# Kernel tuning notes

Hardware: AMD Instinct MI355X
Metric: run time of the kernel (lower is better)

## Reference

```python
import jax, jax.numpy as jnp
import numpy as np

U = 100000   # num_users
I = 100000   # num_items
D = 64       # latent_dim_rec
L = 3        # lightGCN_n_layers
E = 6400000  # number of nonzeros in the sparse adjacency
B = 16384    # batch of (user, item) pairs
N = U + I


def setup_inputs() -> dict:
    key = jax.random.key(0)
    ks = jax.random.split(key, 11)
    return {
        "user_emb": 0.1 * jax.random.normal(ks[0], (U, D), dtype=jnp.float32),
        "item_emb": 0.1 * jax.random.normal(ks[1], (I, D), dtype=jnp.float32),
        "symptom_emb": 0.1 * jax.random.normal(ks[2], (U, D), dtype=jnp.float32),
        "herb_emb": 0.1 * jax.random.normal(ks[3], (I, D), dtype=jnp.float32),
        "user_lw": jax.random.uniform(ks[4], (L + 1,), dtype=jnp.float32),
        "item_lw": jax.random.uniform(ks[5], (L + 1,), dtype=jnp.float32),
        # symmetric-normalized adjacency values are small positive numbers
        "edge_val": jax.random.uniform(ks[6], (E,), dtype=jnp.float32) / 32.0,
        "edge_row": jax.random.randint(ks[7], (E,), 0, N, dtype=jnp.int32),
        "edge_col": jax.random.randint(ks[8], (E,), 0, N, dtype=jnp.int32),
        "users": jax.random.randint(ks[9], (B,), 0, U, dtype=jnp.int32),
        "items": jax.random.randint(ks[10], (B,), 0, I, dtype=jnp.int32),
    }


def _computer(user_emb, item_emb, symptom_emb, herb_emb, user_lw, item_lw,
              edge_val, edge_row, edge_col):
    # layer-0 semantic fusion
    a0 = jax.nn.sigmoid(user_lw[0])
    b0 = jax.nn.sigmoid(item_lw[0])
    u = a0 * user_emb + (1.0 - a0) * symptom_emb
    it = b0 * item_emb + (1.0 - b0) * herb_emb
    all_emb = jnp.concatenate([u, it], axis=0)  # [N, D]
    acc = all_emb  # running sum over layers (mean taken at the end)
    for layer in range(1, L + 1):
        # SpMM: A @ all_emb via gather + segment_sum over edge list
        msg = edge_val[:, None] * all_emb[edge_col]          # [E, D]
        all_emb = jax.ops.segment_sum(msg, edge_row, num_segments=N)
        a = jax.nn.sigmoid(user_lw[layer])
        b = jax.nn.sigmoid(item_lw[layer])
        cu = a * all_emb[:U] + (1.0 - a) * symptom_emb
        ci = b * all_emb[U:] + (1.0 - b) * herb_emb
        all_emb = jnp.concatenate([cu, ci], axis=0)
        acc = acc + all_emb
    light_out = acc / (L + 1)   # mean over stacked layer outputs
    return light_out[:U], light_out[U:]


def reference(user_emb, item_emb, symptom_emb, herb_emb, user_lw, item_lw,
              edge_val, edge_row, edge_col, users, items):
    all_users, all_items = _computer(user_emb, item_emb, symptom_emb, herb_emb,
                                     user_lw, item_lw, edge_val, edge_row, edge_col)
    users_emb = all_users[users]   # [B, D]
    items_emb = all_items[items]   # [B, D]
    gamma = jnp.sum(users_emb * items_emb, axis=1)  # [B]
    return gamma
```

## Files before the change

### kernel.cpp

```cpp
#include <hip/hip_runtime.h>

constexpr int U_N = 100000;
constexpr int I_N = 100000;
constexpr int D   = 64;
constexpr int NL  = 3;
constexpr int NN  = U_N + I_N;
constexpr long long NDLL = (long long)NN * D;
constexpr long long ND4  = NDLL / 4;
constexpr long long UD4  = (long long)U_N * D / 4;

constexpr int BKT_SHIFT = 10;
constexpr int BKT_W     = 1024;
constexpr int NBKT      = (NN + BKT_W - 1) / BKT_W;
constexpr int KSTAGE    = 13;
constexpr int SCHUNK_MAX = KSTAGE * 1024;

typedef float f32x2 __attribute__((ext_vector_type(2)));

__device__ __forceinline__ float sigmoidf_(float x) {
    return 1.0f / (1.0f + expf(-x));
}

__device__ __forceinline__ float bf_lo(unsigned int u) {
    return __uint_as_float(u << 16);
}
__device__ __forceinline__ float bf_hi(unsigned int u) {
    return __uint_as_float(u & 0xFFFF0000u);
}
__device__ __forceinline__ f32x2 bfpair(unsigned int u) {
    f32x2 r;
    r.x = __uint_as_float(u << 16);
    r.y = __uint_as_float(u & 0xFFFF0000u);
    return r;
}
__device__ __forceinline__ unsigned short f2bf(float f) {
    unsigned int u = __float_as_uint(f);
    u += 0x7FFFu + ((u >> 16) & 1u);
    return (unsigned short)(u >> 16);
}
__device__ __forceinline__ unsigned int pack2bf(float lo, float hi) {
    return (unsigned int)f2bf(lo) | ((unsigned int)f2bf(hi) << 16);
}

__global__ void fuse0_bf16_kernel(const float* __restrict__ user_emb,
                                  const float* __restrict__ item_emb,
                                  const float* __restrict__ symptom_emb,
                                  const float* __restrict__ herb_emb,
                                  const float* __restrict__ user_lw,
                                  const float* __restrict__ item_lw,
                                  unsigned short* __restrict__ e0b) {
    long long idx = (long long)blockIdx.x * blockDim.x + threadIdx.x;
    if (idx >= ND4) return;
    float a0 = sigmoidf_(user_lw[0]);
    float b0 = sigmoidf_(item_lw[0]);
    float4 e, s;
    float w;
    if (idx < UD4) {
        e = ((const float4*)user_emb)[idx];
        s = ((const float4*)symptom_emb)[idx];
        w = a0;
    } else {
        long long j = idx - UD4;
        e = ((const float4*)item_emb)[j];
        s = ((const float4*)herb_emb)[j];
        w = b0;
    }
    ushort4 rb;
    rb.x = f2bf(w * e.x + (1.0f - w) * s.x);
    rb.y = f2bf(w * e.y + (1.0f - w) * s.y);
    rb.z = f2bf(w * e.z + (1.0f - w) * s.z);
    rb.w = f2bf(w * e.w + (1.0f - w) * s.w);
    ((ushort4*)e0b)[idx] = rb;
}

__global__ void init_cursor_kernel(int* __restrict__ cursor, int cap) {
    int i = blockIdx.x * blockDim.x + threadIdx.x;
    if (i < NBKT) cursor[i] = i * cap;
}

__global__ void fused_scatter_kernel(const float* __restrict__ edge_val,
                                     const int*   __restrict__ edge_row,
                                     const int*   __restrict__ edge_col,
                                     int* __restrict__ cursor,
                                     int2* __restrict__ binned,
                                     int E, int chunk) {
    __shared__ int h[NBKT];
    int tid = threadIdx.x;
    if (tid < NBKT) h[tid] = 0;
    __syncthreads();
    int s_ = blockIdx.x * chunk;
    int eend = min(E, s_ + chunk);
    int rr[KSTAGE];
    int cc[KSTAGE];
    float vv[KSTAGE];
    #pragma unroll
    for (int k = 0; k < KSTAGE; ++k) {
        int e = s_ + tid + k * 1024;
        bool ok = e < eend;
        rr[k] = ok ? edge_row[e] : -1;
        cc[k] = ok ? edge_col[e] : 0;
        vv[k] = ok ? edge_val[e] : 0.0f;
        if (ok) atomicAdd(&h[rr[k] >> BKT_SHIFT], 1);
    }
    __syncthreads();
    if (tid < NBKT) {
        int c = h[tid];
        if (c) h[tid] = atomicAdd(&cursor[tid], c);
    }
    __syncthreads();
    #pragma unroll
    for (int k = 0; k < KSTAGE; ++k) {
        if (rr[k] >= 0) {
            int b = rr[k] >> BKT_SHIFT;
            int pos = atomicAdd(&h[b], 1);
            binned[pos] = make_int2(__float_as_int(vv[k]),
                                    cc[k] | ((rr[k] & (BKT_W - 1)) << 18));
        }
    }
}

__global__ void bucket_to_csr_kernel(const int2* __restrict__ binned,
                                     const int*  __restrict__ cursor,
                                     int2* __restrict__ row_ptr2,
                                     int2* __restrict__ sorted, int cap) {
    int b = blockIdx.x;
    int start = b * cap;
    int end   = cursor[b];
    __shared__ int rc[BKT_W];
    __shared__ int sm[BKT_W];
    int tid = threadIdx.x;
    rc[tid] = 0;
    __syncthreads();
    for (int e = start + tid; e < end; e += blockDim.x)
        atomicAdd(&rc[(unsigned)binned[e].y >> 18], 1);
    __syncthreads();
    int x = rc[tid];
    sm[tid] = x;
    __syncthreads();
    for (int off = 1; off < BKT_W; off <<= 1) {
        int t = (tid >= off) ? sm[tid - off] : 0;
        __syncthreads();
        sm[tid] += t;
        __syncthreads();
    }
    int excl = sm[tid] - x;
    int gidx = (b << BKT_SHIFT) + tid;
    if (gidx < NN) row_ptr2[gidx] = make_int2(start + excl, start + excl + x);
    __syncthreads();
    rc[tid] = excl;
    __syncthreads();
    for (int e = start + tid; e < end; e += blockDim.x) {
        int2 a = binned[e];
        int rl = (unsigned)a.y >> 18;
        int pos = start + atomicAdd(&rc[rl], 1);
        sorted[pos] = make_int2(a.x, (a.y & 0x3FFFF) << 7);
    }
}

__device__ __forceinline__ void csr_row_sum8(const int2* __restrict__ sorted,
                                             const char* __restrict__ srcB,
                                             int start, int end, unsigned poff,
                                             f32x2 s[4]) {
    #pragma unroll
    for (int j = 0; j < 4; ++j) s[j] = (f32x2){0.f, 0.f};
    int e = start;
    if (e + 8 <= end) {
        int2 a[8];
        #pragma unroll
        for (int k = 0; k < 8; ++k) a[k] = sorted[e + k];
        for (; e + 16 <= end; e += 8) {
            uint4 q[8];
            #pragma unroll
            for (int k = 0; k < 8; ++k)
                q[k] = *(const uint4*)(srcB + (size_t)((unsigned)a[k].y | poff));
            int2 an[8];
            #pragma unroll
            for (int k = 0; k < 8; ++k) an[k] = sorted[e + 8 + k];
            #pragma unroll
            for (int k = 0; k < 8; ++k) {
                f32x2 v; v.x = __int_as_float(a[k].x); v.y = v.x;
                s[0] += v * bfpair(q[k].x);
                s[1] += v * bfpair(q[k].y);
                s[2] += v * bfpair(q[k].z);
                s[3] += v * bfpair(q[k].w);
            }
            #pragma unroll
            for (int k = 0; k < 8; ++k) a[k] = an[k];
        }
        uint4 q[8];
        #pragma unroll
        for (int k = 0; k < 8; ++k)
            q[k] = *(const uint4*)(srcB + (size_t)((unsigned)a[k].y | poff));
        #pragma unroll
        for (int k = 0; k < 8; ++k) {
            f32x2 v; v.x = __int_as_float(a[k].x); v.y = v.x;
            s[0] += v * bfpair(q[k].x);
            s[1] += v * bfpair(q[k].y);
            s[2] += v * bfpair(q[k].z);
            s[3] += v * bfpair(q[k].w);
        }
        e += 8;
    }
    if (e < end) {
        int2 a[8];
        #pragma unroll
        for (int k = 0; k < 8; ++k) {
            int idx = e + k;
            a[k] = sorted[idx < end ? idx : end - 1];
            if (idx >= end) a[k].x = 0;
        }
        uint4 q[8];
        #pragma unroll
        for (int k = 0; k < 8; ++k)
            q[k] = *(const uint4*)(srcB + (size_t)((unsigned)a[k].y | poff));
        #pragma unroll
        for (int k = 0; k < 8; ++k) {
            f32x2 v; v.x = __int_as_float(a[k].x); v.y = v.x;
            s[0] += v * bfpair(q[k].x);
            s[1] += v * bfpair(q[k].y);
            s[2] += v * bfpair(q[k].z);
            s[3] += v * bfpair(q[k].w);
        }
    }
}

__global__ void spmm_csr_full_kernel(const int2* __restrict__ sorted,
                                     const int2* __restrict__ row_ptr2,
                                     const unsigned short* __restrict__ src,
                                     const float* __restrict__ symptom_emb,
                                     const float* __restrict__ herb_emb,
                                     const float* __restrict__ user_lw,
                                     const float* __restrict__ item_lw,
                                     int layer,
                                     unsigned short* __restrict__ dst_b) {
    int wid  = threadIdx.x >> 6;
    int lane = threadIdx.x & 63;
    int r    = lane >> 3;
    int p    = lane & 7;
    int row  = (blockIdx.x * (blockDim.x >> 6) + wid) * 8 + r;
    if (row >= NN) return;
    int2 rp = row_ptr2[row];

    f32x2 s[4];
    csr_row_sum8(sorted, (const char*)src, rp.x, rp.y, (unsigned)(p << 4), s);

    size_t o = ((size_t)row << 6) + ((size_t)p << 3);
    float wgt;
    const float* semp;
    if (row < U_N) {
        wgt = sigmoidf_(user_lw[layer]);
        semp = symptom_emb + o;
    } else {
        wgt = sigmoidf_(item_lw[layer]);
        semp = herb_emb + o - ((size_t)U_N << 6);
    }
    float4 sa = *(const float4*)semp;
    float4 sb = *(const float4*)(semp + 4);
    float om = 1.0f - wgt;
    uint4 ob;
    ob.x = pack2bf(wgt * s[0].x + om * sa.x, wgt * s[0].y + om * sa.y);
    ob.y = pack2bf(wgt * s[1].x + om * sa.z, wgt * s[1].y + om * sa.w);
    ob.z = pack2bf(wgt * s[2].x + om * sb.x, wgt * s[2].y + om * sb.y);
    ob.w = pack2bf(wgt * s[3].x + om * sb.z, wgt * s[3].y + om * sb.w);
    *(uint4*)(dst_b + o) = ob;
}

__global__ void spmm_csr_compact_kernel(const int2* __restrict__ sorted,
                                        const int2* __restrict__ row_ptr2,
                                        const unsigned short* __restrict__ src,
                                        const float* __restrict__ user_emb,
                                        const float* __restrict__ item_emb,
                                        const float* __restrict__ symptom_emb,
                                        const float* __restrict__ herb_emb,
                                        const float* __restrict__ user_lw,
                                        const float* __restrict__ item_lw,
                                        int layer,
                                        const int* __restrict__ users,
                                        const int* __restrict__ items,
                                        const unsigned short* __restrict__ e1b,
                                        const unsigned short* __restrict__ e2b,
                                        float* __restrict__ e3c,
                                        int B) {
    int wid  = threadIdx.x >> 6;
    int lane = threadIdx.x & 63;
    int r    = lane >> 3;
    int p    = lane & 7;
    int b    = (blockIdx.x * (blockDim.x >> 6) + wid) * 8 + r;
    if (b >= 2 * B) return;
    int row = (b < B) ? users[b] : (items[b - B] + U_N);
    int2 rp = row_ptr2[row];

    f32x2 s[4];
    csr_row_sum8(sorted, (const char*)src, rp.x, rp.y, (unsigned)(p << 4), s);

    size_t orow = ((size_t)row << 6) + ((size_t)p << 3);
    float wgt, w0;
    const float* semp;
    const float* embp;
    if (row < U_N) {
        wgt = sigmoidf_(user_lw[layer]);
        w0  = sigmoidf_(user_lw[0]);
        semp = symptom_emb + orow;
        embp = user_emb + orow;
    } else {
        size_t ol = orow - ((size_t)U_N << 6);
        wgt = sigmoidf_(item_lw[layer]);
        w0  = sigmoidf_(item_lw[0]);
        semp = herb_emb + ol;
        embp = item_emb + ol;
    }
    float4 sa = *(const float4*)semp;
    float4 sb = *(const float4*)(semp + 4);
    float4 ea = *(const float4*)embp;
    float4 eb = *(const float4*)(embp + 4);
    uint4 q1 = ((const uint4*)e1b)[((size_t)row << 3) + p];
    uint4 q2 = ((const uint4*)e2b)[((size_t)row << 3) + p];
    float om = 1.0f - wgt, om0 = 1.0f - w0;
    float4 ra, rb;
    ra.x = (w0 * ea.x + om0 * sa.x) + bf_lo(q1.x) + bf_lo(q2.x)
         + (wgt * s[0].x + om * sa.x);
    ra.y = (w0 * ea.y + om0 * sa.y) + bf_hi(q1.x) + bf_hi(q2.x)
         + (wgt * s[0].y + om * sa.y);
    ra.z = (w0 * ea.z + om0 * sa.z) + bf_lo(q1.y) + bf_lo(q2.y)
         + (wgt * s[1].x + om * sa.z);
    ra.w = (w0 * ea.w + om0 * sa.w) + bf_hi(q1.y) + bf_hi(q2.y)
         + (wgt * s[1].y + om * sa.w);
    rb.x = (w0 * eb.x + om0 * sb.x) + bf_lo(q1.z) + bf_lo(q2.z)
         + (wgt * s[2].x + om * sb.x);
    rb.y = (w0 * eb.y + om0 * sb.y) + bf_hi(q1.z) + bf_hi(q2.z)
         + (wgt * s[2].y + om * sb.y);
    rb.z = (w0 * eb.z + om0 * sb.z) + bf_lo(q1.w) + bf_lo(q2.w)
         + (wgt * s[3].x + om * sb.z);
    rb.w = (w0 * eb.w + om0 * sb.w) + bf_hi(q1.w) + bf_hi(q2.w)
         + (wgt * s[3].y + om * sb.w);
    float* op = e3c + ((size_t)b << 6) + ((size_t)p << 3);
    *(float4*)op = ra;
    *(float4*)(op + 4) = rb;
}

__global__ void gamma_kernel(const float* __restrict__ e3c,
                             float* __restrict__ out,
                             int B) {
    int gtid = blockIdx.x * blockDim.x + threadIdx.x;
    int wid  = gtid >> 6;
    int lane = threadIdx.x & 63;
    if (wid >= B) return;
    float su = e3c[((size_t)wid << 6) | lane];
    float si = e3c[((size_t)(B + wid) << 6) | lane];
    float pr = su * si;
    #pragma unroll
    for (int off = 32; off > 0; off >>= 1)
        pr += __shfl_down(pr, off, 64);
    if (lane == 0) out[wid] = pr * (1.0f / 16.0f);
}

__global__ void fuse0_kernel(const float* __restrict__ user_emb,
                             const float* __restrict__ item_emb,
                             const float* __restrict__ symptom_emb,
                             const float* __restrict__ herb_emb,
                             const float* __restrict__ user_lw,
                             const float* __restrict__ item_lw,
                             float* __restrict__ bufA,
                             float* __restrict__ acc,
                             float* __restrict__ bufB) {
    long long idx = (long long)blockIdx.x * blockDim.x + threadIdx.x;
    if (idx >= ND4) return;
    float a0 = sigmoidf_(user_lw[0]);
    float b0 = sigmoidf_(item_lw[0]);
    float4 e, s;
    float w;
    if (idx < UD4) {
        e = ((const float4*)user_emb)[idx];
        s = ((const float4*)symptom_emb)[idx];
        w = a0;
    } else {
        long long j = idx - UD4;
        e = ((const float4*)item_emb)[j];
        s = ((const float4*)herb_emb)[j];
        w = b0;
    }
    float4 r;
    r.x = w * e.x + (1.0f - w) * s.x;
    r.y = w * e.y + (1.0f - w) * s.y;
    r.z = w * e.z + (1.0f - w) * s.z;
    r.w = w * e.w + (1.0f - w) * s.w;
    ((float4*)bufA)[idx] = r;
    ((float4*)acc)[idx]  = r;
    float4 z; z.x = z.y = z.z = z.w = 0.0f;
    ((float4*)bufB)[idx] = z;
}

__global__ void spmm_scatter_kernel(const float* __restrict__ edge_val,
                                    const int*   __restrict__ edge_row,
                                    const int*   __restrict__ edge_col,
                                    const float* __restrict__ src,
                                    float*       __restrict__ dst,
                                    long long total) {
    long long idx = (long long)blockIdx.x * blockDim.x + threadIdx.x;
    if (idx >= total) return;
    long long e = idx >> 4;
    int       q = (int)(idx & 15);
    int r = edge_row[e];
    int c = edge_col[e];
    float v = edge_val[e];
    float4 x = *(const float4*)(src + (long long)c * D + q * 4);
    float* d = dst + (long long)r * D + q * 4;
    atomicAdd(d + 0, v * x.x);
    atomicAdd(d + 1, v * x.y);
    atomicAdd(d + 2, v * x.z);
    atomicAdd(d + 3, v * x.w);
}

__global__ void fuse_layer_kernel(const float* __restrict__ symptom_emb,
                                  const float* __restrict__ herb_emb,
                                  const float* __restrict__ user_lw,
                                  const float* __restrict__ item_lw,
                                  int layer,
                                  float* __restrict__ bufA,
                                  float* __restrict__ bufB,
                                  float* __restrict__ acc) {
    long long idx = (long long)blockIdx.x * blockDim.x + threadIdx.x;
    if (idx >= ND4) return;
    float a = sigmoidf_(user_lw[layer]);
    float b = sigmoidf_(item_lw[layer]);
    float4 m = ((float4*)bufB)[idx];
    float4 z; z.x = z.y = z.z = z.w = 0.0f;
    ((float4*)bufB)[idx] = z;
    float4 s;
    float w;
    if (idx < UD4) {
        s = ((const float4*)symptom_emb)[idx];
        w = a;
    } else {
        s = ((const float4*)herb_emb)[idx - UD4];
        w = b;
    }
    float4 r;
    r.x = w * m.x + (1.0f - w) * s.x;
    r.y = w * m.y + (1.0f - w) * s.y;
    r.z = w * m.z + (1.0f - w) * s.z;
    r.w = w * m.w + (1.0f - w) * s.w;
    ((float4*)bufA)[idx] = r;
    float4 ac = ((float4*)acc)[idx];
    ac.x += r.x; ac.y += r.y; ac.z += r.z; ac.w += r.w;
    ((float4*)acc)[idx] = ac;
}

__global__ void gamma_acc_kernel(const float* __restrict__ acc,
                                 const int* __restrict__ users,
                                 const int* __restrict__ items,
                                 float* __restrict__ out,
                                 int B) {
    int gtid = blockIdx.x * blockDim.x + threadIdx.x;
    int wid  = gtid >> 6;
    int lane = threadIdx.x & 63;
    if (wid >= B) return;
    int u  = users[wid];
    int it = items[wid];
    float su = acc[(long long)u * D + lane];
    float si = acc[((long long)(U_N + it)) * D + lane];
    float p = su * si;
    #pragma unroll
    for (int off = 32; off > 0; off >>= 1)
        p += __shfl_down(p, off, 64);
    if (lane == 0) out[wid] = p * (1.0f / 16.0f);
}

extern "C" void kernel_launch(void* const* d_in, const int* in_sizes, int n_in,
                              void* d_out, int out_size, void* d_ws, size_t ws_size,
                              hipStream_t stream) {
    const float* user_emb    = (const float*)d_in[0];
    const float* item_emb    = (const float*)d_in[1];
    const float* symptom_emb = (const float*)d_in[2];
    const float* herb_emb    = (const float*)d_in[3];
    const float* user_lw     = (const float*)d_in[4];
    const float* item_lw     = (const float*)d_in[5];
    const float* edge_val    = (const float*)d_in[6];
    const int*   edge_row    = (const int*)d_in[7];
    const int*   edge_col    = (const int*)d_in[8];
    const int*   users       = (const int*)d_in[9];
    const int*   items       = (const int*)d_in[10];
    float* out = (float*)d_out;

    const int E = in_sizes[6];
    const int B = in_sizes[9];
    const int TPB = 256;

    int ablk2 = (E + 12499) / 12500;
    int chunk = (E + ablk2 - 1) / ablk2;
    int cap = E / NBKT + E / NBKT / 16 + 1024;
    size_t slab_bytes = (size_t)NBKT * cap * 8;

    size_t off = 0;
    auto carve = [&](size_t bytes) -> char* {
        char* p = (char*)d_ws + off;
        off += (bytes + 255) & ~(size_t)255;
        return p;
    };
    unsigned short* e0b     = (unsigned short*)carve(NDLL * 2);
    unsigned short* e1b     = (unsigned short*)carve(NDLL * 2);
    int2*           binned  = (int2*)carve(slab_bytes);
    int2*           sorted  = (int2*)carve(slab_bytes);
    int2*           row_ptr2= (int2*)carve((size_t)NN * 8);
    int*            cursor  = (int*)carve((size_t)NBKT * 4);
    const size_t fast_bytes = off;
    unsigned short* e2b = e0b;
    float*          e3c = (float*)binned;

    if (ws_size >= fast_bytes && slab_bytes >= (size_t)2 * B * D * 4
        && chunk <= SCHUNK_MAX) {
        int fb = (int)((ND4 + TPB - 1) / TPB);
        fuse0_bf16_kernel<<<fb, TPB, 0, stream>>>(user_emb, item_emb, symptom_emb,
                                                  herb_emb, user_lw, item_lw, e0b);

        init_cursor_kernel<<<1, 256, 0, stream>>>(cursor, cap);
        fused_scatter_kernel<<<ablk2, 1024, 0, stream>>>(edge_val, edge_row,
                                                         edge_col, cursor,
                                                         binned, E, chunk);
        bucket_to_csr_kernel<<<NBKT, BKT_W, 0, stream>>>(binned, cursor,
                                                         row_ptr2, sorted, cap);

        int sblocks = (NN + 31) / 32;
        spmm_csr_full_kernel<<<sblocks, TPB, 0, stream>>>(
            sorted, row_ptr2, e0b, symptom_emb, herb_emb,
            user_lw, item_lw, 1, e1b);
        spmm_csr_full_kernel<<<sblocks, TPB, 0, stream>>>(
            sorted, row_ptr2, e1b, symptom_emb, herb_emb,
            user_lw, item_lw, 2, e2b);
        int cblocks = (2 * B + 31) / 32;
        spmm_csr_compact_kernel<<<cblocks, TPB, 0, stream>>>(
            sorted, row_ptr2, e2b, user_emb, item_emb, symptom_emb, herb_emb,
            user_lw, item_lw, 3, users, items, e1b, e2b, e3c, B);

        int gblocks = (B * 64 + TPB - 1) / TPB;
        gamma_kernel<<<gblocks, TPB, 0, stream>>>(e3c, out, B);
    } else {
        float* bufA = (float*)d_ws;
        float* bufB = bufA + NDLL;
        float* acc2 = bufB + NDLL;

        int fb = (int)((ND4 + TPB - 1) / TPB);
        fuse0_kernel<<<fb, TPB, 0, stream>>>(user_emb, item_emb, symptom_emb,
                                             herb_emb, user_lw, item_lw,
                                             bufA, acc2, bufB);
        for (int layer = 1; layer <= NL; ++layer) {
            long long total = (long long)E * 16;
            int blocks = (int)((total + TPB - 1) / TPB);
            spmm_scatter_kernel<<<blocks, TPB, 0, stream>>>(edge_val, edge_row,
                                                            edge_col, bufA, bufB,
                                                            total);
            int fblocks = (int)((ND4 + TPB - 1) / TPB);
            fuse_layer_kernel<<<fblocks, TPB, 0, stream>>>(symptom_emb, herb_emb,
                                                           user_lw, item_lw, layer,
                                                           bufA, bufB, acc2);
        }
        int gblocks = (B * 64 + TPB - 1) / TPB;
        gamma_acc_kernel<<<gblocks, TPB, 0, stream>>>(acc2, users, items, out, B);
    }
}
```

Measured before the change: 571.3 us.

## Order SpMM rows by descending degree via a counting-sort permutation

```diff
diff --git a/kernel.cpp b/kernel.cpp
--- a/kernel.cpp
+++ b/kernel.cpp
@@ -14,6 +14,7 @@
 constexpr int NBKT      = (NN + BKT_W - 1) / BKT_W;
 constexpr int KSTAGE    = 13;
 constexpr int SCHUNK_MAX = KSTAGE * 1024;
+constexpr int DBINS     = 1024;
 
 typedef float f32x2 __attribute__((ext_vector_type(2)));
 
@@ -154,6 +155,70 @@
         int rl = (unsigned)a.y >> 18;
         int pos = start + atomicAdd(&rc[rl], 1);
         sorted[pos] = make_int2(a.x, (a.y & 0x3FFFF) << 7);
+    }
+}
+
+__global__ void zero_hist_kernel(int* __restrict__ hist) {
+    hist[threadIdx.x] = 0;
+}
+
+__global__ void deg_hist_kernel(const int2* __restrict__ row_ptr2,
+                                int* __restrict__ hist) {
+    __shared__ int h[DBINS];
+    int tid = threadIdx.x;
+    h[tid] = 0;
+    __syncthreads();
+    int i = blockIdx.x * 1024 + tid;
+    if (i < NN) {
+        int2 rp = row_ptr2[i];
+        int d = min(rp.y - rp.x, DBINS - 1);
+        atomicAdd(&h[DBINS - 1 - d], 1);
+    }
+    __syncthreads();
+    int c = h[tid];
+    if (c) atomicAdd(&hist[tid], c);
+}
+
+__global__ void scan_hist_kernel(const int* __restrict__ hist,
+                                 int* __restrict__ cur) {
+    __shared__ int sm[DBINS];
+    int tid = threadIdx.x;
+    int x = hist[tid];
+    sm[tid] = x;
+    __syncthreads();
+    for (int off = 1; off < DBINS; off <<= 1) {
+        int t = (tid >= off) ? sm[tid - off] : 0;
+        __syncthreads();
+        sm[tid] += t;
+        __syncthreads();
+    }
+    cur[tid] = sm[tid] - x;
+}
+
+__global__ void perm_scatter_kernel(const int2* __restrict__ row_ptr2,
+                                    int* __restrict__ cur,
+                                    int* __restrict__ perm) {
+    __shared__ int h[DBINS];
+    __shared__ int base_[DBINS];
+    int tid = threadIdx.x;
+    h[tid] = 0;
+    __syncthreads();
+    int i = blockIdx.x * 1024 + tid;
+    int bin = -1;
+    if (i < NN) {
+        int2 rp = row_ptr2[i];
+        int d = min(rp.y - rp.x, DBINS - 1);
+        bin = DBINS - 1 - d;
+        atomicAdd(&h[bin], 1);
+    }
+    __syncthreads();
+    int c = h[tid];
+    base_[tid] = c ? atomicAdd(&cur[tid], c) : 0;
+    h[tid] = 0;
+    __syncthreads();
+    if (i < NN) {
+        int loc = atomicAdd(&h[bin], 1);
+        perm[base_[bin] + loc] = i;
     }
 }
 
@@ -226,6 +291,7 @@
 
 __global__ void spmm_csr_full_kernel(const int2* __restrict__ sorted,
                                      const int2* __restrict__ row_ptr2,
+                                     const int*  __restrict__ perm,
                                      const unsigned short* __restrict__ src,
                                      const float* __restrict__ symptom_emb,
                                      const float* __restrict__ herb_emb,
@@ -237,9 +303,10 @@
     int lane = threadIdx.x & 63;
     int r    = lane >> 3;
     int p    = lane & 7;
-    int row  = (blockIdx.x * (blockDim.x >> 6) + wid) * 8 + r;
-    if (row >= NN) return;
-    int2 rp = row_ptr2[row];
+    int slot = (blockIdx.x * (blockDim.x >> 6) + wid) * 8 + r;
+    if (slot >= NN) return;
+    int row  = perm[slot];
+    int2 rp  = row_ptr2[row];
 
     f32x2 s[4];
     csr_row_sum8(sorted, (const char*)src, rp.x, rp.y, (unsigned)(p << 4), s);
@@ -503,6 +570,9 @@
     int2*           sorted  = (int2*)carve(slab_bytes);
     int2*           row_ptr2= (int2*)carve((size_t)NN * 8);
     int*            cursor  = (int*)carve((size_t)NBKT * 4);
+    int*            perm    = (int*)carve((size_t)NN * 4);
+    int*            dhist   = (int*)carve((size_t)DBINS * 4);
+    int*            dcur    = (int*)carve((size_t)DBINS * 4);
     const size_t fast_bytes = off;
     unsigned short* e2b = e0b;
     float*          e3c = (float*)binned;
@@ -520,12 +590,18 @@
         bucket_to_csr_kernel<<<NBKT, BKT_W, 0, stream>>>(binned, cursor,
                                                          row_ptr2, sorted, cap);
 
+        int pblocks = (NN + 1023) / 1024;
+        zero_hist_kernel<<<1, DBINS, 0, stream>>>(dhist);
+        deg_hist_kernel<<<pblocks, 1024, 0, stream>>>(row_ptr2, dhist);
+        scan_hist_kernel<<<1, DBINS, 0, stream>>>(dhist, dcur);
+        perm_scatter_kernel<<<pblocks, 1024, 0, stream>>>(row_ptr2, dcur, perm);
+
         int sblocks = (NN + 31) / 32;
         spmm_csr_full_kernel<<<sblocks, TPB, 0, stream>>>(
-            sorted, row_ptr2, e0b, symptom_emb, herb_emb,
+            sorted, row_ptr2, perm, e0b, symptom_emb, herb_emb,
             user_lw, item_lw, 1, e1b);
         spmm_csr_full_kernel<<<sblocks, TPB, 0, stream>>>(
-            sorted, row_ptr2, e1b, symptom_emb, herb_emb,
+            sorted, row_ptr2, perm, e1b, symptom_emb, herb_emb,
             user_lw, item_lw, 2, e2b);
         int cblocks = (2 * B + 31) / 32;
         spmm_csr_compact_kernel<<<cblocks, TPB, 0, stream>>>(
```

Measured after the change: 588.6 us. +3.0%, slower.

## Shrink buckets to 256 rows and sort edges in LDS before coalesced CSR write

Applied to the files above, without the earlier changes.

```diff
diff --git a/kernel.cpp b/kernel.cpp
--- a/kernel.cpp
+++ b/kernel.cpp
@@ -9,9 +9,10 @@
 constexpr long long ND4  = NDLL / 4;
 constexpr long long UD4  = (long long)U_N * D / 4;
 
-constexpr int BKT_SHIFT = 10;
-constexpr int BKT_W     = 1024;
+constexpr int BKT_SHIFT = 8;
+constexpr int BKT_W     = 256;
 constexpr int NBKT      = (NN + BKT_W - 1) / BKT_W;
+constexpr int CAP_MAX   = 9216;
 constexpr int KSTAGE    = 13;
 constexpr int SCHUNK_MAX = KSTAGE * 1024;
 
@@ -123,37 +124,49 @@
                                      const int*  __restrict__ cursor,
                                      int2* __restrict__ row_ptr2,
                                      int2* __restrict__ sorted, int cap) {
+    __shared__ int2 eds[CAP_MAX];
+    __shared__ int  inv[CAP_MAX];
+    __shared__ int  rc[BKT_W];
+    __shared__ int  sm[BKT_W];
     int b = blockIdx.x;
     int start = b * cap;
-    int end   = cursor[b];
-    __shared__ int rc[BKT_W];
-    __shared__ int sm[BKT_W];
+    int cnt   = cursor[b] - start;
+    if (cnt > CAP_MAX) cnt = CAP_MAX;
     int tid = threadIdx.x;
-    rc[tid] = 0;
-    __syncthreads();
-    for (int e = start + tid; e < end; e += blockDim.x)
-        atomicAdd(&rc[(unsigned)binned[e].y >> 18], 1);
-    __syncthreads();
-    int x = rc[tid];
-    sm[tid] = x;
+    if (tid < BKT_W) rc[tid] = 0;
+    __syncthreads();
+    for (int i = tid; i < cnt; i += 1024) {
+        int2 a = binned[start + i];
+        eds[i] = a;
+        atomicAdd(&rc[(unsigned)a.y >> 18], 1);
+    }
+    __syncthreads();
+    int x = 0;
+    if (tid < BKT_W) { x = rc[tid]; sm[tid] = x; }
     __syncthreads();
     for (int off = 1; off < BKT_W; off <<= 1) {
-        int t = (tid >= off) ? sm[tid - off] : 0;
+        int t = (tid >= off && tid < BKT_W) ? sm[tid - off] : 0;
         __syncthreads();
-        sm[tid] += t;
+        if (tid < BKT_W) sm[tid] += t;
         __syncthreads();
     }
-    int excl = sm[tid] - x;
-    int gidx = (b << BKT_SHIFT) + tid;
-    if (gidx < NN) row_ptr2[gidx] = make_int2(start + excl, start + excl + x);
-    __syncthreads();
-    rc[tid] = excl;
-    __syncthreads();
-    for (int e = start + tid; e < end; e += blockDim.x) {
-        int2 a = binned[e];
-        int rl = (unsigned)a.y >> 18;
-        int pos = start + atomicAdd(&rc[rl], 1);
-        sorted[pos] = make_int2(a.x, (a.y & 0x3FFFF) << 7);
+    if (tid < BKT_W) {
+        int excl = sm[tid] - x;
+        int gidx = (b << BKT_SHIFT) + tid;
+        if (gidx < NN)
+            row_ptr2[gidx] = make_int2(start + excl, start + excl + x);
+        rc[tid] = excl;
+    }
+    __syncthreads();
+    for (int i = tid; i < cnt; i += 1024) {
+        int rl  = (unsigned)eds[i].y >> 18;
+        int pos = atomicAdd(&rc[rl], 1);
+        inv[pos] = i;
+    }
+    __syncthreads();
+    for (int t_ = tid; t_ < cnt; t_ += 1024) {
+        int2 a = eds[inv[t_]];
+        sorted[start + t_] = make_int2(a.x, (a.y & 0x3FFFF) << 7);
     }
 }
 
@@ -488,7 +501,7 @@
 
     int ablk2 = (E + 12499) / 12500;
     int chunk = (E + ablk2 - 1) / ablk2;
-    int cap = E / NBKT + E / NBKT / 16 + 1024;
+    int cap = E / NBKT + E / NBKT / 32 + 512;
     size_t slab_bytes = (size_t)NBKT * cap * 8;
 
     size_t off = 0;
@@ -508,17 +521,17 @@
     float*          e3c = (float*)binned;
 
     if (ws_size >= fast_bytes && slab_bytes >= (size_t)2 * B * D * 4
-        && chunk <= SCHUNK_MAX) {
+        && chunk <= SCHUNK_MAX && cap <= CAP_MAX) {
         int fb = (int)((ND4 + TPB - 1) / TPB);
         fuse0_bf16_kernel<<<fb, TPB, 0, stream>>>(user_emb, item_emb, symptom_emb,
                                                   herb_emb, user_lw, item_lw, e0b);
 
-        init_cursor_kernel<<<1, 256, 0, stream>>>(cursor, cap);
+        init_cursor_kernel<<<(NBKT + 255) / 256, 256, 0, stream>>>(cursor, cap);
         fused_scatter_kernel<<<ablk2, 1024, 0, stream>>>(edge_val, edge_row,
                                                          edge_col, cursor,
                                                          binned, E, chunk);
-        bucket_to_csr_kernel<<<NBKT, BKT_W, 0, stream>>>(binned, cursor,
-                                                         row_ptr2, sorted, cap);
+        bucket_to_csr_kernel<<<NBKT, 1024, 0, stream>>>(binned, cursor,
+                                                        row_ptr2, sorted, cap);
 
         int sblocks = (NN + 31) / 32;
         spmm_csr_full_kernel<<<sblocks, TPB, 0, stream>>>(
```

Result: faster. 556.4 us (-2.6%).
